# Performance work log

Hardware: AMD Instinct MI355X
Metric: run time of the kernel (lower is better)

Reference implementation:

```python
import jax, jax.numpy as jnp
import numpy as np

B, N, C, NS = 4, 2048, 128, 64
RADIUS = 0.25
BN_EPS = 1e-5


def _ball_query(xyz):
    """First-NS point indices within RADIUS of each point (pointnet2 semantics:
    indices taken in ascending point order, short balls padded with the first hit).
    xyz: (B,N,3) -> idx: (B,N,NS) int32."""
    sq = jnp.sum(xyz * xyz, axis=-1)                                   # (B,N)
    d2 = sq[:, :, None] + sq[:, None, :] - 2.0 * jnp.einsum('bnd,bmd->bnm', xyz, xyz)
    within = d2 < RADIUS ** 2                                          # (B,N,N)
    cand = jnp.where(within, jnp.arange(N, dtype=jnp.int32)[None, None, :], N)
    idx = jnp.sort(cand, axis=-1)[..., :NS]                            # first NS hits
    idx = jnp.where(idx == N, idx[..., :1], idx)                       # pad with first hit
    return idx


def _bn_relu(h, g, b):
    # eval-mode BatchNorm2d with running_mean=0, running_var=1, then ReLU
    inv = 1.0 / jnp.sqrt(1.0 + BN_EPS)
    return jax.nn.relu(g[None, :, None, None] * (h * inv) + b[None, :, None, None])


def _forward(xyz, features, W1, W2, W3, g1, g2, g3, b1, b2, b3):
    idx = _ball_query(xyz)                                             # (B,N,NS)
    bidx = jnp.arange(B)[:, None, None]
    g_xyz = xyz[bidx, idx]                                             # (B,N,NS,3)
    grouped_xyz = jnp.transpose(g_xyz - xyz[:, :, None, :], (0, 3, 1, 2))  # (B,3,N,NS) relative
    feat_t = jnp.transpose(features, (0, 2, 1))                        # (B,N,C)
    g_feat = jnp.transpose(feat_t[bidx, idx], (0, 3, 1, 2))            # (B,C,N,NS)
    grouped_features = jnp.concatenate([grouped_xyz, g_feat], axis=1)  # (B,3+C,N,NS)

    xyz_feature = jnp.concatenate([jnp.transpose(xyz, (0, 2, 1)), features], axis=1)  # (B,3+C,N)
    center = jax.lax.stop_gradient(xyz_feature)[..., None]             # .detach() in torch
    diff = grouped_features - center
    h = diff * diff                                                    # squared diff

    h = _bn_relu(jnp.einsum('oc,bcns->bons', W1, h), g1, b1)           # (B,256,N,NS)
    h = _bn_relu(jnp.einsum('oc,bcns->bons', W2, h), g2, b2)           # (B,128,N,NS)
    h = _bn_relu(jnp.einsum('oc,bcns->bons', W3, h), g3, b3)           # (B,1,N,NS)

    shift = jnp.sum(grouped_xyz * h, axis=-1)                          # (B,3,N)
    return shift / jnp.sum(h, axis=-1)                                 # / (B,1,N)


def setup_inputs() -> dict:
    key = jax.random.key(0)
    ks = jax.random.split(key, 5)
    cin = C + 3
    return {
        'xyz': jax.random.uniform(ks[0], (B, N, 3), dtype=jnp.float32),
        'features': jax.random.normal(ks[1], (B, C, N), dtype=jnp.float32),
        'W1': jax.random.normal(ks[2], (256, cin), dtype=jnp.float32) * np.float32(np.sqrt(2.0 / cin)),
        'W2': jax.random.normal(ks[3], (128, 256), dtype=jnp.float32) * np.float32(np.sqrt(2.0 / 256)),
        'W3': jax.random.normal(ks[4], (1, 128), dtype=jnp.float32) * np.float32(np.sqrt(2.0 / 128)),
        'g1': jnp.ones((256,), jnp.float32), 'g2': jnp.ones((128,), jnp.float32), 'g3': jnp.ones((1,), jnp.float32),
        'b1': jnp.zeros((256,), jnp.float32), 'b2': jnp.zeros((128,), jnp.float32), 'b3': jnp.zeros((1,), jnp.float32),
    }


def reference(xyz, features, W1, W2, W3, g1, g2, g3, b1, b2, b3):
    return _forward(xyz, features, W1, W2, W3, g1, g2, g3, b1, b2, b3)
```

## Files before the change

### kernel.cpp

```cpp
#include <hip/hip_runtime.h>
#include <math.h>

typedef _Float16 f16;
typedef _Float16 f16x8 __attribute__((ext_vector_type(8)));
typedef _Float16 f16x4 __attribute__((ext_vector_type(4)));
typedef float f32x4 __attribute__((ext_vector_type(4)));

#define B_  4
#define N_  2048
#define C_  128
#define NS_ 64

#define WS_FEAT16 0u
#define WS_IDX    2097152u
#define WS_W1X    3145728u
#define WS_W1P    3153920u
#define WS_W2P    3219456u

#define OFF_H   0
#define OFF_HX  16384
#define OFF_W   18432
#define OFF_A2  0
#define OFF_GX  51200
#define OFF_QF  51968
#define OFF_IDX 52480
#define OFF_RED 52480
#define OFF_W3  52736
#define LDS_TOTAL 53248

__device__ __forceinline__ void gl_lds16(const char* gp, char* lp) {
  __builtin_amdgcn_global_load_lds(
      (const __attribute__((address_space(1))) unsigned int*)gp,
      (__attribute__((address_space(3))) unsigned int*)lp, 16, 0, 0);
}

__device__ __forceinline__ unsigned pk2(float a, float b) {
  union { f16 h[2]; unsigned u; } cv;
  cv.h[0] = (f16)a; cv.h[1] = (f16)b;
  return cv.u;
}

__global__ __launch_bounds__(256) void prep_kernel(
    const float* __restrict__ feat, const float* __restrict__ W1,
    const float* __restrict__ W2,
    const float* __restrict__ g1, const float* __restrict__ g2,
    f16* __restrict__ feat16,
    char* __restrict__ W1x, char* __restrict__ W1p, char* __restrict__ W2p)
{
  const float inv = 1.0f / sqrtf(1.0f + 1e-5f);
  int i = blockIdx.x * 256 + threadIdx.x;
  {
    int n = i & (N_ - 1);
    int bc = i >> 11;
    int c = bc & (C_ - 1);
    int b = bc >> 7;
    feat16[(size_t)((b << 11) + n) * C_ + c] = (f16)feat[i];
  }
  if (i < 16384) {
    int g = i >> 12, r = i & 4095, o = r >> 4, j = r & 15;
    float sc = g1[o] * inv;
    const float* row = W1 + o * 131 + 3 + g * 32 + 2 * j;
    unsigned byte = ((unsigned)(o * 64 + j * 4)) ^ ((unsigned)(((o >> 1) & 7) << 4));
    *(unsigned*)(W1p + (size_t)g * 16384 + byte) = pk2(row[0] * sc, row[1] * sc);
  }
  if (i < 16384) {
    int ko = i >> 12, r = i & 4095, p = r >> 5, j = r & 31;
    float sc = g2[p] * inv;
    int o = ko * 64 + 2 * j;
    unsigned byte = ((unsigned)(p * 128 + j * 4)) ^ ((unsigned)((p & 7) << 4));
    *(unsigned*)(W2p + (size_t)ko * 16384 + byte) =
        pk2(W2[p * 256 + o] * sc, W2[p * 256 + o + 1] * sc);
  }
  if (i < 2048) {
    int o = i >> 3, j = i & 7;
    float sc = g1[o] * inv;
    unsigned v = 0;
    if (j == 0)      v = pk2(W1[o * 131 + 0] * sc, W1[o * 131 + 1] * sc);
    else if (j == 1) v = pk2(W1[o * 131 + 2] * sc, 0.0f);
    *(unsigned*)(W1x + o * 32 + j * 4) = v;
  }
}

__global__ __launch_bounds__(256) void ballquery_kernel(
    const float* __restrict__ xyz, unsigned short* __restrict__ idxout)
{
  __shared__ float  xl[N_ * 3];
  __shared__ double sq[N_];
  __shared__ int    ibuf[4][NS_];

  const int b  = blockIdx.x >> 9;
  const int ng = blockIdx.x & 511;
  const int t  = threadIdx.x;
  const float* xb = xyz + (size_t)b * N_ * 3;

  for (int i = t; i < N_ * 3; i += 256) xl[i] = xb[i];
  __syncthreads();
  for (int i = t; i < N_; i += 256) {
    double x = (double)xl[3*i], y = (double)xl[3*i+1], z = (double)xl[3*i+2];
    sq[i] = x*x + y*y + z*z;
  }
  __syncthreads();

  const int wv = t >> 6, lane = t & 63;
  const int n = ng * 4 + wv;
  const double xn = (double)xl[3*n], yn = (double)xl[3*n+1], zn = (double)xl[3*n+2];
  const double sn = sq[n];

  int cnt = 0;
  for (int mb = 0; mb < N_; mb += 64) {
    int m = mb + lane;
    double dot = xn*(double)xl[3*m] + yn*(double)xl[3*m+1] + zn*(double)xl[3*m+2];
    double d2 = (sn + sq[m]) - 2.0 * dot;
    bool hit = d2 < 0.0625;
    unsigned long long mask = __ballot(hit);
    int pos = __popcll(mask & ((1ULL << lane) - 1ULL));
    int slot = cnt + pos;
    if (hit && slot < NS_) ibuf[wv][slot] = m;
    cnt += (int)__popcll(mask);
    if (cnt >= NS_) break;
  }
  asm volatile("s_waitcnt lgkmcnt(0)" ::: "memory");
  int total = cnt < NS_ ? cnt : NS_;
  int v = ibuf[wv][lane < total ? lane : 0];
  idxout[((size_t)b * N_ + n) * NS_ + lane] = (unsigned short)v;
}

__global__ __launch_bounds__(256, 3) void mlp_kernel(
    const float* __restrict__ xyz, const f16* __restrict__ feat16,
    const char* __restrict__ w1x, const char* __restrict__ w1p,
    const char* __restrict__ w2p,
    const unsigned short* __restrict__ idxg,
    const float* __restrict__ W3g,
    const float* __restrict__ b1,
    const float* __restrict__ b2,
    const float* __restrict__ g3, const float* __restrict__ b3,
    float* __restrict__ out)
{
  __shared__ __attribute__((aligned(128))) char lds[LDS_TOTAL];

  const int bidRaw = blockIdx.x;
  const int bn = ((bidRaw & 7) << 10) + (bidRaw >> 3);
  const int b = bn >> 11;
  const int n = bn & (N_ - 1);
  const int t = threadIdx.x;
  const int w = t >> 6, lane = t & 63;
  const int l15 = lane & 15, lg = lane >> 4;
  const unsigned swzl = (unsigned)(((l15 >> 1) & 7) << 4);
  const unsigned labase = ((unsigned)(l15 * 64 + lg * 16)) ^ swzl;
  const unsigned swz2 = (unsigned)((l15 & 7) << 4);
  const unsigned w2b0 = ((unsigned)(l15 * 128 + lg * 16)) ^ swz2;
  const unsigned w2b1 = ((unsigned)(l15 * 128 + 64 + lg * 16)) ^ swz2;
  const float inv = 1.0f / sqrtf(1.0f + 1e-5f);

  float bo1v[4];
  #pragma unroll
  for (int nt = 0; nt < 4; ++nt) {
    int o = (nt >> 1) * 128 + 32 * w + (nt & 1) * 16 + l15;
    bo1v[nt] = b1[o];
  }
  float bo2v[2];
  #pragma unroll
  for (int nt = 0; nt < 2; ++nt) {
    int p = 32 * w + nt * 16 + l15;
    bo2v[nt] = b2[p];
  }
  const float g3c = g3[0] * inv, b3c = b3[0];
  const float xn0 = xyz[(size_t)bn*3+0], xn1 = xyz[(size_t)bn*3+1], xn2 = xyz[(size_t)bn*3+2];

  auto STAGE = [&](int sl) {
    const char* gp; int nloads;
    if (sl == 0)      { gp = w1x;                          nloads = 2; }
    else if (sl <= 4) { gp = w1p + (size_t)(sl - 1) * 16384; nloads = 4; }
    else              { gp = w2p + (size_t)(sl - 5) * 16384; nloads = 4; }
    gp += t * 16;
    char* lp = lds + OFF_W + ((sl & 1) << 14) + (w << 10);
    for (int i = 0; i < nloads; ++i)
      gl_lds16(gp + i * 4096, lp + i * 4096);
  };

  f32x4 acc1[4][4];
  f32x4 acc2[4][2];
  #pragma unroll
  for (int mt = 0; mt < 4; ++mt)
    #pragma unroll
    for (int nt2 = 0; nt2 < 2; ++nt2) {
      f32x4 c = {bo2v[nt2], bo2v[nt2], bo2v[nt2], bo2v[nt2]};
      acc2[mt][nt2] = c;
    }

  STAGE(0);
  if (t < 64) ((int*)(lds + OFF_IDX))[t] = (int)idxg[(size_t)bn * 64 + t];
  if (t < 64) ((unsigned*)(lds + OFF_QF))[t] =
      ((const unsigned*)(feat16 + (size_t)bn * C_))[t];
  if (t < 128) ((float*)(lds + OFF_W3))[t] = W3g[t] * g3c;
  __syncthreads();

  const int* idxl = (const int*)(lds + OFF_IDX);

  {
    int s = t & 63, g = t >> 6;
    int m = idxl[s];
    const f16* pb = feat16 + ((size_t)b * N_ + m) * C_ + g * 32;
    const f16* qb = (const f16*)(lds + OFF_QF) + g * 32;
    const unsigned sw = ((unsigned)((s >> 1) & 7)) << 4;
    const unsigned base = (unsigned)(g * 4096);
    #pragma unroll
    for (int qq = 0; qq < 4; ++qq) {
      f16x8 p = *(const f16x8*)(pb + qq * 8);
      f16x8 q = *(const f16x8*)(qb + qq * 8);
      f16x8 d = p - q;
      f16x8 hh = d * d;
      unsigned byte = base
        + ((((unsigned)(s * 64 + qq * 16)) ^ sw ^ ((unsigned)((g & 3) << 4))));
      *(f16x8*)(lds + OFF_H + byte) = hh;
    }
  }
  if (t < 64) {
    int s = t;
    int m = idxl[s];
    const float* pm = xyz + ((size_t)b * N_ + m) * 3;
    float p0 = pm[0], p1 = pm[1], p2c = pm[2];
    float* gxp = (float*)(lds + OFF_GX) + s * 3;
    gxp[0] = p0 - xn0; gxp[1] = p1 - xn1; gxp[2] = p2c - xn2;
    float h0 = p0 - 2.0f * xn0; h0 *= h0;
    float h1 = p1 - 2.0f * xn1; h1 *= h1;
    float h2 = p2c - 2.0f * xn2; h2 *= h2;
    char* hx = lds + OFF_HX + s * 32;
    *(unsigned*)(hx + 0)  = pk2(h0, h1);
    *(unsigned*)(hx + 4)  = pk2(h2, 0.0f);
    *(unsigned*)(hx + 8)  = 0u;
    *(unsigned*)(hx + 12) = 0u;
    f32x4 z4 = {0.0f, 0.0f, 0.0f, 0.0f};
    *(f32x4*)(hx + 16) = z4;
  }

  asm volatile("s_waitcnt vmcnt(0) lgkmcnt(0)" ::: "memory");
  __builtin_amdgcn_s_barrier();
  STAGE(1);
  {
    const char* wbx = lds + OFF_W;
    f16x4 bf4[4];
    #pragma unroll
    for (int nt = 0; nt < 4; ++nt) {
      int orow = (nt >> 1) * 128 + 32 * w + (nt & 1) * 16 + l15;
      bf4[nt] = *(const f16x4*)(wbx + orow * 32 + lg * 8);
    }
    f16x4 af4[4];
    #pragma unroll
    for (int mt = 0; mt < 4; ++mt)
      af4[mt] = *(const f16x4*)(lds + OFF_HX + (16 * mt + l15) * 32 + lg * 8);
    #pragma unroll
    for (int mt = 0; mt < 4; ++mt)
      #pragma unroll
      for (int nt = 0; nt < 4; ++nt) {
        f32x4 cb = {bo1v[nt], bo1v[nt], bo1v[nt], bo1v[nt]};
        acc1[mt][nt] = __builtin_amdgcn_mfma_f32_16x16x16f16(af4[mt], bf4[nt], cb, 0, 0, 0);
      }
  }

  #pragma unroll
  for (int g = 0; g < 4; ++g) {
    const int sl = 1 + g;
    asm volatile("s_waitcnt vmcnt(0) lgkmcnt(0)" ::: "memory");
    __builtin_amdgcn_s_barrier();
    STAGE(sl + 1);
    const char* wb = lds + OFF_W + ((sl & 1) << 14);
    f16x8 bf[4];
    #pragma unroll
    for (int nt = 0; nt < 4; ++nt) {
      int ob = (nt >> 1) * 128 + 32 * w + (nt & 1) * 16;
      bf[nt] = *(const f16x8*)(wb + ob * 64 + labase);
    }
    const char* hb = lds + OFF_H + g * 4096;
    const unsigned gx4 = ((unsigned)g) << 4;
    f16x8 af[4];
    #pragma unroll
    for (int mt = 0; mt < 4; ++mt)
      af[mt] = *(const f16x8*)(hb + mt * 1024 + (labase ^ gx4));
    __builtin_amdgcn_s_setprio(1);
    #pragma unroll
    for (int mt = 0; mt < 4; ++mt)
      #pragma unroll
      for (int nt = 0; nt < 4; ++nt)
        acc1[mt][nt] = __builtin_amdgcn_mfma_f32_16x16x32_f16(af[mt], bf[nt], acc1[mt][nt], 0, 0, 0);
    __builtin_amdgcn_s_setprio(0);
  }

  auto EPI1 = [&](int hf) {
    #pragma unroll
    for (int mt = 0; mt < 4; ++mt)
      #pragma unroll
      for (int nt2 = 0; nt2 < 2; ++nt2) {
        const int nt = hf * 2 + nt2;
        #pragma unroll
        for (int r = 0; r < 4; ++r) {
          int s = mt * 16 + lg * 4 + r;
          float a = acc1[mt][nt][r];
          a = a > 0.0f ? a : 0.0f;
          unsigned byte = (unsigned)(w * 4096)
            + (((unsigned)(s * 64 + nt2 * 32 + l15 * 2)) ^ ((unsigned)(((s >> 1) & 7) << 4))
               ^ ((unsigned)((w & 3) << 4)));
          *(f16*)(lds + OFF_H + byte) = (f16)a;
        }
      }
  };
  asm volatile("s_waitcnt lgkmcnt(0)" ::: "memory");
  __builtin_amdgcn_s_barrier();
  EPI1(0);

  #pragma unroll
  for (int k = 0; k < 4; ++k) {
    const int sl = 5 + k;
    asm volatile("s_waitcnt vmcnt(0) lgkmcnt(0)" ::: "memory");
    __builtin_amdgcn_s_barrier();
    if (sl < 8) STAGE(sl + 1);
    const char* wb = lds + OFF_W + ((sl & 1) << 14);
    f16x8 bq0[2], bq1[2];
    #pragma unroll
    for (int nt2 = 0; nt2 < 2; ++nt2) {
      int pb = (32 * w + nt2 * 16) * 128;
      bq0[nt2] = *(const f16x8*)(wb + pb + w2b0);
      bq1[nt2] = *(const f16x8*)(wb + pb + w2b1);
    }
    const int sl0 = (2 * k) & 3, sl1 = (2 * k + 1) & 3;
    f16x8 a0f[4], a1f[4];
    #pragma unroll
    for (int mt = 0; mt < 4; ++mt) {
      a0f[mt] = *(const f16x8*)(lds + OFF_H + sl0 * 4096 + mt * 1024 + (labase ^ (unsigned)(sl0 << 4)));
      a1f[mt] = *(const f16x8*)(lds + OFF_H + sl1 * 4096 + mt * 1024 + (labase ^ (unsigned)(sl1 << 4)));
    }
    __builtin_amdgcn_s_setprio(1);
    #pragma unroll
    for (int mt = 0; mt < 4; ++mt)
      #pragma unroll
      for (int nt2 = 0; nt2 < 2; ++nt2) {
        f32x4 c = acc2[mt][nt2];
        c = __builtin_amdgcn_mfma_f32_16x16x32_f16(a0f[mt], bq0[nt2], c, 0, 0, 0);
        c = __builtin_amdgcn_mfma_f32_16x16x32_f16(a1f[mt], bq1[nt2], c, 0, 0, 0);
        acc2[mt][nt2] = c;
      }
    __builtin_amdgcn_s_setprio(0);
    if (k == 1) {
      asm volatile("s_waitcnt lgkmcnt(0)" ::: "memory");
      __builtin_amdgcn_s_barrier();
      EPI1(1);
    }
  }
  asm volatile("s_waitcnt lgkmcnt(0)" ::: "memory");
  __builtin_amdgcn_s_barrier();

  #pragma unroll
  for (int mt = 0; mt < 4; ++mt)
    #pragma unroll
    for (int nt2 = 0; nt2 < 2; ++nt2) {
      int p2 = 32 * w + nt2 * 16 + l15;
      #pragma unroll
      for (int r = 0; r < 4; ++r) {
        int s = mt * 16 + lg * 4 + r;
        float a = acc2[mt][nt2][r];
        a = a > 0.0f ? a : 0.0f;
        *(float*)(lds + OFF_A2 + s * 528 + p2 * 4) = a;
      }
    }
  asm volatile("s_waitcnt lgkmcnt(0)" ::: "memory");
  __builtin_amdgcn_s_barrier();

  {
    int s3 = t >> 2, q3 = t & 3;
    const float* a2row = (const float*)(lds + OFF_A2) + s3 * 132;
    const float* w3r = (const float*)(lds + OFF_W3);
    float z3 = 0.0f;
    #pragma unroll
    for (int i = 0; i < 8; ++i) {
      f32x4 av = *(const f32x4*)(a2row + q3 * 32 + i * 4);
      f32x4 wv = *(const f32x4*)(w3r + q3 * 32 + i * 4);
      z3 = fmaf(av[0], wv[0], z3); z3 = fmaf(av[1], wv[1], z3);
      z3 = fmaf(av[2], wv[2], z3); z3 = fmaf(av[3], wv[3], z3);
    }
    z3 += __shfl_xor(z3, 1);
    z3 += __shfl_xor(z3, 2);
    float wgt = z3 + b3c;
    wgt = wgt > 0.0f ? wgt : 0.0f;
    float v0 = 0.f, v1 = 0.f, v2 = 0.f, v3 = 0.f;
    if (q3 == 0) {
      const float* gx = (const float*)(lds + OFF_GX) + s3 * 3;
      v0 = gx[0] * wgt; v1 = gx[1] * wgt; v2 = gx[2] * wgt; v3 = wgt;
    }
    #pragma unroll
    for (int off = 4; off < 64; off <<= 1) {
      v0 += __shfl_xor(v0, off); v1 += __shfl_xor(v1, off);
      v2 += __shfl_xor(v2, off); v3 += __shfl_xor(v3, off);
    }
    if (lane == 0) {
      float* red = (float*)(lds + OFF_RED);
      red[w * 4 + 0] = v0; red[w * 4 + 1] = v1;
      red[w * 4 + 2] = v2; red[w * 4 + 3] = v3;
    }
    __syncthreads();
    if (t == 0) {
      const float* red = (const float*)(lds + OFF_RED);
      float n0 = red[0] + red[4] + red[8]  + red[12];
      float n1 = red[1] + red[5] + red[9]  + red[13];
      float n2 = red[2] + red[6] + red[10] + red[14];
      float dd = red[3] + red[7] + red[11] + red[15];
      out[(size_t)(b * 3 + 0) * N_ + n] = n0 / dd;
      out[(size_t)(b * 3 + 1) * N_ + n] = n1 / dd;
      out[(size_t)(b * 3 + 2) * N_ + n] = n2 / dd;
    }
  }
}

extern "C" void kernel_launch(void* const* d_in, const int* in_sizes, int n_in,
                              void* d_out, int out_size, void* d_ws, size_t ws_size,
                              hipStream_t stream) {
  (void)in_sizes; (void)n_in; (void)out_size; (void)ws_size;
  const float* xyz      = (const float*)d_in[0];
  const float* features = (const float*)d_in[1];
  const float* W1 = (const float*)d_in[2];
  const float* W2 = (const float*)d_in[3];
  const float* W3 = (const float*)d_in[4];
  const float* g1 = (const float*)d_in[5];
  const float* g2 = (const float*)d_in[6];
  const float* g3 = (const float*)d_in[7];
  const float* b1 = (const float*)d_in[8];
  const float* b2 = (const float*)d_in[9];
  const float* b3 = (const float*)d_in[10];
  float* out = (float*)d_out;

  char* ws = (char*)d_ws;
  f16* feat16         = (f16*)(ws + WS_FEAT16);
  unsigned short* idx = (unsigned short*)(ws + WS_IDX);
  char* W1x           = ws + WS_W1X;
  char* W1p           = ws + WS_W1P;
  char* W2p           = ws + WS_W2P;

  prep_kernel<<<dim3((B_ * C_ * N_) / 256), dim3(256), 0, stream>>>(
      features, W1, W2, g1, g2, feat16, W1x, W1p, W2p);
  ballquery_kernel<<<dim3(B_ * N_ / 4), dim3(256), 0, stream>>>(xyz, idx);
  mlp_kernel<<<dim3(B_ * N_), dim3(256), 0, stream>>>(
      xyz, feat16, W1x, W1p, W2p, idx, W3, b1, b2, g3, b3, out);
}
```

Baseline: 136.3 us.

## Fuse layer-3 dot product into MFMA accumulators and drop prologue LDS staging

The final 128-to-1 projection is now computed directly from the layer-2 MFMA accumulator registers using per-lane W3 values and xor-shuffle reductions. This replaces writing the full activation tile to LDS, synchronising, and rereading it, so one barrier and a large LDS round trip are removed. The prologue also loads the neighbour indices and centre features straight from global memory per thread instead of staging them through LDS behind a __syncthreads. In exchange, each thread does more shuffle work, and the prologue issues redundant global reads.

```diff
diff --git a/kernel.cpp b/kernel.cpp
--- a/kernel.cpp
+++ b/kernel.cpp
@@ -20,12 +20,8 @@
 #define OFF_H   0
 #define OFF_HX  16384
 #define OFF_W   18432
-#define OFF_A2  0
 #define OFF_GX  51200
-#define OFF_QF  51968
-#define OFF_IDX 52480
-#define OFF_RED 52480
-#define OFF_W3  52736
+#define OFF_Z3  51968
 #define LDS_TOTAL 53248
 
 __device__ __forceinline__ void gl_lds16(const char* gp, char* lp) {
@@ -165,6 +161,8 @@
     bo2v[nt] = b2[p];
   }
   const float g3c = g3[0] * inv, b3c = b3[0];
+  const float w3a = W3g[32 * w + l15] * g3c;
+  const float w3b = W3g[32 * w + 16 + l15] * g3c;
   const float xn0 = xyz[(size_t)bn*3+0], xn1 = xyz[(size_t)bn*3+1], xn2 = xyz[(size_t)bn*3+2];
 
   auto STAGE = [&](int sl) {
@@ -189,21 +187,14 @@
     }
 
   STAGE(0);
-  if (t < 64) ((int*)(lds + OFF_IDX))[t] = (int)idxg[(size_t)bn * 64 + t];
-  if (t < 64) ((unsigned*)(lds + OFF_QF))[t] =
-      ((const unsigned*)(feat16 + (size_t)bn * C_))[t];
-  if (t < 128) ((float*)(lds + OFF_W3))[t] = W3g[t] * g3c;
-  __syncthreads();
-
-  const int* idxl = (const int*)(lds + OFF_IDX);
+  const int s_me = t & 63, g_me = t >> 6;
+  const int m_me = (int)idxg[(size_t)bn * 64 + s_me];
 
   {
-    int s = t & 63, g = t >> 6;
-    int m = idxl[s];
-    const f16* pb = feat16 + ((size_t)b * N_ + m) * C_ + g * 32;
-    const f16* qb = (const f16*)(lds + OFF_QF) + g * 32;
-    const unsigned sw = ((unsigned)((s >> 1) & 7)) << 4;
-    const unsigned base = (unsigned)(g * 4096);
+    const f16* pb = feat16 + ((size_t)b * N_ + m_me) * C_ + g_me * 32;
+    const f16* qb = feat16 + (size_t)bn * C_ + g_me * 32;
+    const unsigned sw = ((unsigned)((s_me >> 1) & 7)) << 4;
+    const unsigned base = (unsigned)(g_me * 4096);
     #pragma unroll
     for (int qq = 0; qq < 4; ++qq) {
       f16x8 p = *(const f16x8*)(pb + qq * 8);
@@ -211,21 +202,19 @@
       f16x8 d = p - q;
       f16x8 hh = d * d;
       unsigned byte = base
-        + ((((unsigned)(s * 64 + qq * 16)) ^ sw ^ ((unsigned)((g & 3) << 4))));
+        + ((((unsigned)(s_me * 64 + qq * 16)) ^ sw ^ ((unsigned)((g_me & 3) << 4))));
       *(f16x8*)(lds + OFF_H + byte) = hh;
     }
   }
   if (t < 64) {
-    int s = t;
-    int m = idxl[s];
-    const float* pm = xyz + ((size_t)b * N_ + m) * 3;
+    const float* pm = xyz + ((size_t)b * N_ + m_me) * 3;
     float p0 = pm[0], p1 = pm[1], p2c = pm[2];
-    float* gxp = (float*)(lds + OFF_GX) + s * 3;
+    float* gxp = (float*)(lds + OFF_GX) + s_me * 3;
     gxp[0] = p0 - xn0; gxp[1] = p1 - xn1; gxp[2] = p2c - xn2;
     float h0 = p0 - 2.0f * xn0; h0 *= h0;
     float h1 = p1 - 2.0f * xn1; h1 *= h1;
     float h2 = p2c - 2.0f * xn2; h2 *= h2;
-    char* hx = lds + OFF_HX + s * 32;
+    char* hx = lds + OFF_HX + s_me * 32;
     *(unsigned*)(hx + 0)  = pk2(h0, h1);
     *(unsigned*)(hx + 4)  = pk2(h2, 0.0f);
     *(unsigned*)(hx + 8)  = 0u;
@@ -346,66 +335,51 @@
       EPI1(1);
     }
   }
+
+  {
+    float pz[4][4];
+    #pragma unroll
+    for (int mt = 0; mt < 4; ++mt)
+      #pragma unroll
+      for (int r = 0; r < 4; ++r) {
+        float a0 = acc2[mt][0][r]; a0 = a0 > 0.0f ? a0 : 0.0f;
+        float a1 = acc2[mt][1][r]; a1 = a1 > 0.0f ? a1 : 0.0f;
+        pz[mt][r] = fmaf(a0, w3a, a1 * w3b);
+      }
+    #pragma unroll
+    for (int off = 1; off < 16; off <<= 1)
+      #pragma unroll
+      for (int mt = 0; mt < 4; ++mt)
+        #pragma unroll
+        for (int r = 0; r < 4; ++r)
+          pz[mt][r] += __shfl_xor(pz[mt][r], off);
+    if (l15 == 0) {
+      float* z3p = (float*)(lds + OFF_Z3) + w * 64;
+      #pragma unroll
+      for (int mt = 0; mt < 4; ++mt)
+        #pragma unroll
+        for (int r = 0; r < 4; ++r)
+          z3p[mt * 16 + lg * 4 + r] = pz[mt][r];
+    }
+  }
   asm volatile("s_waitcnt lgkmcnt(0)" ::: "memory");
   __builtin_amdgcn_s_barrier();
 
-  #pragma unroll
-  for (int mt = 0; mt < 4; ++mt)
-    #pragma unroll
-    for (int nt2 = 0; nt2 < 2; ++nt2) {
-      int p2 = 32 * w + nt2 * 16 + l15;
-      #pragma unroll
-      for (int r = 0; r < 4; ++r) {
-        int s = mt * 16 + lg * 4 + r;
-        float a = acc2[mt][nt2][r];
-        a = a > 0.0f ? a : 0.0f;
-        *(float*)(lds + OFF_A2 + s * 528 + p2 * 4) = a;
-      }
-    }
-  asm volatile("s_waitcnt lgkmcnt(0)" ::: "memory");
-  __builtin_amdgcn_s_barrier();
-
-  {
-    int s3 = t >> 2, q3 = t & 3;
-    const float* a2row = (const float*)(lds + OFF_A2) + s3 * 132;
-    const float* w3r = (const float*)(lds + OFF_W3);
-    float z3 = 0.0f;
-    #pragma unroll
-    for (int i = 0; i < 8; ++i) {
-      f32x4 av = *(const f32x4*)(a2row + q3 * 32 + i * 4);
-      f32x4 wv = *(const f32x4*)(w3r + q3 * 32 + i * 4);
-      z3 = fmaf(av[0], wv[0], z3); z3 = fmaf(av[1], wv[1], z3);
-      z3 = fmaf(av[2], wv[2], z3); z3 = fmaf(av[3], wv[3], z3);
-    }
-    z3 += __shfl_xor(z3, 1);
-    z3 += __shfl_xor(z3, 2);
-    float wgt = z3 + b3c;
-    wgt = wgt > 0.0f ? wgt : 0.0f;
-    float v0 = 0.f, v1 = 0.f, v2 = 0.f, v3 = 0.f;
-    if (q3 == 0) {
-      const float* gx = (const float*)(lds + OFF_GX) + s3 * 3;
-      v0 = gx[0] * wgt; v1 = gx[1] * wgt; v2 = gx[2] * wgt; v3 = wgt;
-    }
-    #pragma unroll
-    for (int off = 4; off < 64; off <<= 1) {
+  if (t < 64) {
+    const float* z3p = (const float*)(lds + OFF_Z3);
+    float z3 = z3p[t] + z3p[64 + t] + z3p[128 + t] + z3p[192 + t] + b3c;
+    float wgt = z3 > 0.0f ? z3 : 0.0f;
+    const float* gx = (const float*)(lds + OFF_GX) + t * 3;
+    float v0 = gx[0] * wgt, v1 = gx[1] * wgt, v2 = gx[2] * wgt, v3 = wgt;
+    #pragma unroll
+    for (int off = 1; off < 64; off <<= 1) {
       v0 += __shfl_xor(v0, off); v1 += __shfl_xor(v1, off);
       v2 += __shfl_xor(v2, off); v3 += __shfl_xor(v3, off);
     }
-    if (lane == 0) {
-      float* red = (float*)(lds + OFF_RED);
-      red[w * 4 + 0] = v0; red[w * 4 + 1] = v1;
-      red[w * 4 + 2] = v2; red[w * 4 + 3] = v3;
-    }
-    __syncthreads();
     if (t == 0) {
-      const float* red = (const float*)(lds + OFF_RED);
-      float n0 = red[0] + red[4] + red[8]  + red[12];
-      float n1 = red[1] + red[5] + red[9]  + red[13];
-      float n2 = red[2] + red[6] + red[10] + red[14];
-      float dd = red[3] + red[7] + red[11] + red[15];
-      out[(size_t)(b * 3 + 0) * N_ + n] = n0 / dd;
-      out[(size_t)(b * 3 + 1) * N_ + n] = n1 / dd;
-      out[(size_t)(b * 3 + 2) * N_ + n] = n2 / dd;
+      out[(size_t)(b * 3 + 0) * N_ + n] = v0 / v3;
+      out[(size_t)(b * 3 + 1) * N_ + n] = v1 / v3;
+      out[(size_t)(b * 3 + 2) * N_ + n] = v2 / v3;
     }
   }
 }
```

Result: slower. 143.9 us (+5.6%).

## Read MLP weights directly from global memory instead of LDS staging

Applied to the files above, without the earlier changes.

Removes the double-buffered global_load_lds staging of W1/W2 weight tiles into shared memory. MFMA B-operands are now loaded directly from global (L2-resident) memory, and the swizzle in the prep kernel's weight layout is dropped. This cuts LDS from about 53KB to 35KB per block, which could allow more resident blocks per CU and removes the per-slice barriers. The cost is a global-load latency on every slice with no prefetch, and extra barriers added around the EPI1 stages. W3 is also read from global, with the g3 scale applied after the dot product.

```diff
diff --git a/kernel.cpp b/kernel.cpp
--- a/kernel.cpp
+++ b/kernel.cpp
@@ -19,20 +19,12 @@
 
 #define OFF_H   0
 #define OFF_HX  16384
-#define OFF_W   18432
 #define OFF_A2  0
-#define OFF_GX  51200
-#define OFF_QF  51968
-#define OFF_IDX 52480
-#define OFF_RED 52480
-#define OFF_W3  52736
-#define LDS_TOTAL 53248
-
-__device__ __forceinline__ void gl_lds16(const char* gp, char* lp) {
-  __builtin_amdgcn_global_load_lds(
-      (const __attribute__((address_space(1))) unsigned int*)gp,
-      (__attribute__((address_space(3))) unsigned int*)lp, 16, 0, 0);
-}
+#define OFF_GX  33792
+#define OFF_QF  34560
+#define OFF_IDX 35072
+#define OFF_RED 35328
+#define LDS_TOTAL 35840
 
 __device__ __forceinline__ unsigned pk2(float a, float b) {
   union { f16 h[2]; unsigned u; } cv;
@@ -60,15 +52,14 @@
     int g = i >> 12, r = i & 4095, o = r >> 4, j = r & 15;
     float sc = g1[o] * inv;
     const float* row = W1 + o * 131 + 3 + g * 32 + 2 * j;
-    unsigned byte = ((unsigned)(o * 64 + j * 4)) ^ ((unsigned)(((o >> 1) & 7) << 4));
-    *(unsigned*)(W1p + (size_t)g * 16384 + byte) = pk2(row[0] * sc, row[1] * sc);
+    *(unsigned*)(W1p + (size_t)g * 16384 + o * 64 + j * 4) =
+        pk2(row[0] * sc, row[1] * sc);
   }
   if (i < 16384) {
     int ko = i >> 12, r = i & 4095, p = r >> 5, j = r & 31;
     float sc = g2[p] * inv;
     int o = ko * 64 + 2 * j;
-    unsigned byte = ((unsigned)(p * 128 + j * 4)) ^ ((unsigned)((p & 7) << 4));
-    *(unsigned*)(W2p + (size_t)ko * 16384 + byte) =
+    *(unsigned*)(W2p + (size_t)ko * 16384 + p * 128 + j * 4) =
         pk2(W2[p * 256 + o] * sc, W2[p * 256 + o + 1] * sc);
   }
   if (i < 2048) {
@@ -147,9 +138,9 @@
   const int l15 = lane & 15, lg = lane >> 4;
   const unsigned swzl = (unsigned)(((l15 >> 1) & 7) << 4);
   const unsigned labase = ((unsigned)(l15 * 64 + lg * 16)) ^ swzl;
-  const unsigned swz2 = (unsigned)((l15 & 7) << 4);
-  const unsigned w2b0 = ((unsigned)(l15 * 128 + lg * 16)) ^ swz2;
-  const unsigned w2b1 = ((unsigned)(l15 * 128 + 64 + lg * 16)) ^ swz2;
+  const unsigned gb1 = (unsigned)(l15 * 64 + lg * 16);
+  const unsigned gb20 = (unsigned)(l15 * 128 + lg * 16);
+  const unsigned gb21 = (unsigned)(l15 * 128 + 64 + lg * 16);
   const float inv = 1.0f / sqrtf(1.0f + 1e-5f);
 
   float bo1v[4];
@@ -167,17 +158,6 @@
   const float g3c = g3[0] * inv, b3c = b3[0];
   const float xn0 = xyz[(size_t)bn*3+0], xn1 = xyz[(size_t)bn*3+1], xn2 = xyz[(size_t)bn*3+2];
 
-  auto STAGE = [&](int sl) {
-    const char* gp; int nloads;
-    if (sl == 0)      { gp = w1x;                          nloads = 2; }
-    else if (sl <= 4) { gp = w1p + (size_t)(sl - 1) * 16384; nloads = 4; }
-    else              { gp = w2p + (size_t)(sl - 5) * 16384; nloads = 4; }
-    gp += t * 16;
-    char* lp = lds + OFF_W + ((sl & 1) << 14) + (w << 10);
-    for (int i = 0; i < nloads; ++i)
-      gl_lds16(gp + i * 4096, lp + i * 4096);
-  };
-
   f32x4 acc1[4][4];
   f32x4 acc2[4][2];
   #pragma unroll
@@ -188,11 +168,9 @@
       acc2[mt][nt2] = c;
     }
 
-  STAGE(0);
   if (t < 64) ((int*)(lds + OFF_IDX))[t] = (int)idxg[(size_t)bn * 64 + t];
   if (t < 64) ((unsigned*)(lds + OFF_QF))[t] =
       ((const unsigned*)(feat16 + (size_t)bn * C_))[t];
-  if (t < 128) ((float*)(lds + OFF_W3))[t] = W3g[t] * g3c;
   __syncthreads();
 
   const int* idxl = (const int*)(lds + OFF_IDX);
@@ -233,19 +211,16 @@
     f32x4 z4 = {0.0f, 0.0f, 0.0f, 0.0f};
     *(f32x4*)(hx + 16) = z4;
   }
-
-  asm volatile("s_waitcnt vmcnt(0) lgkmcnt(0)" ::: "memory");
+  asm volatile("s_waitcnt lgkmcnt(0)" ::: "memory");
   __builtin_amdgcn_s_barrier();
-  STAGE(1);
+
   {
-    const char* wbx = lds + OFF_W;
-    f16x4 bf4[4];
+    f16x4 bf4[4], af4[4];
     #pragma unroll
     for (int nt = 0; nt < 4; ++nt) {
       int orow = (nt >> 1) * 128 + 32 * w + (nt & 1) * 16 + l15;
-      bf4[nt] = *(const f16x4*)(wbx + orow * 32 + lg * 8);
-    }
-    f16x4 af4[4];
+      bf4[nt] = *(const f16x4*)(w1x + orow * 32 + lg * 8);
+    }
     #pragma unroll
     for (int mt = 0; mt < 4; ++mt)
       af4[mt] = *(const f16x4*)(lds + OFF_HX + (16 * mt + l15) * 32 + lg * 8);
@@ -257,23 +232,17 @@
         acc1[mt][nt] = __builtin_amdgcn_mfma_f32_16x16x16f16(af4[mt], bf4[nt], cb, 0, 0, 0);
       }
   }
-
   #pragma unroll
   for (int g = 0; g < 4; ++g) {
-    const int sl = 1 + g;
-    asm volatile("s_waitcnt vmcnt(0) lgkmcnt(0)" ::: "memory");
-    __builtin_amdgcn_s_barrier();
-    STAGE(sl + 1);
-    const char* wb = lds + OFF_W + ((sl & 1) << 14);
-    f16x8 bf[4];
+    const char* wbg = w1p + (size_t)g * 16384;
+    f16x8 bf[4], af[4];
     #pragma unroll
     for (int nt = 0; nt < 4; ++nt) {
       int ob = (nt >> 1) * 128 + 32 * w + (nt & 1) * 16;
-      bf[nt] = *(const f16x8*)(wb + ob * 64 + labase);
+      bf[nt] = *(const f16x8*)(wbg + ob * 64 + gb1);
     }
     const char* hb = lds + OFF_H + g * 4096;
     const unsigned gx4 = ((unsigned)g) << 4;
-    f16x8 af[4];
     #pragma unroll
     for (int mt = 0; mt < 4; ++mt)
       af[mt] = *(const f16x8*)(hb + mt * 1024 + (labase ^ gx4));
@@ -307,20 +276,18 @@
   asm volatile("s_waitcnt lgkmcnt(0)" ::: "memory");
   __builtin_amdgcn_s_barrier();
   EPI1(0);
+  asm volatile("s_waitcnt lgkmcnt(0)" ::: "memory");
+  __builtin_amdgcn_s_barrier();
 
   #pragma unroll
   for (int k = 0; k < 4; ++k) {
-    const int sl = 5 + k;
-    asm volatile("s_waitcnt vmcnt(0) lgkmcnt(0)" ::: "memory");
-    __builtin_amdgcn_s_barrier();
-    if (sl < 8) STAGE(sl + 1);
-    const char* wb = lds + OFF_W + ((sl & 1) << 14);
+    const char* wbg = w2p + (size_t)k * 16384;
     f16x8 bq0[2], bq1[2];
     #pragma unroll
     for (int nt2 = 0; nt2 < 2; ++nt2) {
-      int pb = (32 * w + nt2 * 16) * 128;
-      bq0[nt2] = *(const f16x8*)(wb + pb + w2b0);
-      bq1[nt2] = *(const f16x8*)(wb + pb + w2b1);
+      int pb2 = (32 * w + nt2 * 16) * 128;
+      bq0[nt2] = *(const f16x8*)(wbg + pb2 + gb20);
+      bq1[nt2] = *(const f16x8*)(wbg + pb2 + gb21);
     }
     const int sl0 = (2 * k) & 3, sl1 = (2 * k + 1) & 3;
     f16x8 a0f[4], a1f[4];
@@ -344,6 +311,8 @@
       asm volatile("s_waitcnt lgkmcnt(0)" ::: "memory");
       __builtin_amdgcn_s_barrier();
       EPI1(1);
+      asm volatile("s_waitcnt lgkmcnt(0)" ::: "memory");
+      __builtin_amdgcn_s_barrier();
     }
   }
   asm volatile("s_waitcnt lgkmcnt(0)" ::: "memory");
@@ -368,18 +337,17 @@
   {
     int s3 = t >> 2, q3 = t & 3;
     const float* a2row = (const float*)(lds + OFF_A2) + s3 * 132;
-    const float* w3r = (const float*)(lds + OFF_W3);
     float z3 = 0.0f;
     #pragma unroll
     for (int i = 0; i < 8; ++i) {
       f32x4 av = *(const f32x4*)(a2row + q3 * 32 + i * 4);
-      f32x4 wv = *(const f32x4*)(w3r + q3 * 32 + i * 4);
+      f32x4 wv = *(const f32x4*)(W3g + q3 * 32 + i * 4);
       z3 = fmaf(av[0], wv[0], z3); z3 = fmaf(av[1], wv[1], z3);
       z3 = fmaf(av[2], wv[2], z3); z3 = fmaf(av[3], wv[3], z3);
     }
     z3 += __shfl_xor(z3, 1);
     z3 += __shfl_xor(z3, 2);
-    float wgt = z3 + b3c;
+    float wgt = fmaf(z3, g3c, b3c);
     wgt = wgt > 0.0f ? wgt : 0.0f;
     float v0 = 0.f, v1 = 0.f, v2 = 0.f, v3 = 0.f;
     if (q3 == 0) {
```

New measurement: 170.9 us. 1.25x slower.
